# Kernel tuning notes

Measured on AMD Instinct MI355X. Metric: run time of the kernel, lower is better.

The kernel has to match this reference:

```python
import jax, jax.numpy as jnp
import numpy as np

NUM_SPARSE = 26
VOCAB = 100000
EMB = 64
B = 2048
DENSE = 13
NUM_FEA = NUM_SPARSE + 1  # 26 embeddings + bottom-MLP output


def _xavier(key, shape):
    fan_in, fan_out = shape[0], shape[1]
    lim = jnp.sqrt(6.0 / (fan_in + fan_out))
    return jax.random.uniform(key, shape, jnp.float32, -lim, lim)


def setup_inputs() -> dict:
    key = jax.random.key(0)
    ks = jax.random.split(key, 20)
    inp = {
        "dense": jax.random.normal(ks[0], (B, DENSE), jnp.float32),
        "cat_idx": jax.random.randint(ks[1], (B, NUM_SPARSE), 0, VOCAB, jnp.int32),
        # stacked EmbeddingBag tables (all same vocab -> one [26, V, 64] tensor)
        "tables": _xavier(ks[2], (VOCAB, EMB))[None] * jnp.ones((NUM_SPARSE, 1, 1), jnp.float32) * 0
                  + jax.random.normal(ks[3], (NUM_SPARSE, VOCAB, EMB), jnp.float32) * 0.01,
        # bottom MLP: 13 -> 512 -> 256 -> 64
        "bw0": _xavier(ks[4], (DENSE, 512)), "bb0": jnp.zeros((512,), jnp.float32),
        "bw1": _xavier(ks[5], (512, 256)),   "bb1": jnp.zeros((256,), jnp.float32),
        "bw2": _xavier(ks[6], (256, EMB)),   "bb2": jnp.zeros((EMB,), jnp.float32),
        # top MLP: 415 -> 1024 -> 512 -> 256 -> 1
        "tw0": _xavier(ks[7], (EMB + NUM_FEA * (NUM_FEA - 1) // 2, 1024)), "tb0": jnp.zeros((1024,), jnp.float32),
        "tw1": _xavier(ks[8], (1024, 512)),  "tb1": jnp.zeros((512,), jnp.float32),
        "tw2": _xavier(ks[9], (512, 256)),   "tb2": jnp.zeros((256,), jnp.float32),
        "tw3": _xavier(ks[10], (256, 1)),    "tb3": jnp.zeros((1,), jnp.float32),
    }
    return inp


def reference(dense, cat_idx, tables, bw0, bb0, bw1, bb1, bw2, bb2,
              tw0, tb0, tw1, tb1, tw2, tb2, tw3, tb3):
    # bottom MLP on dense features -> [B, EMB]
    h = jax.nn.relu(dense @ bw0 + bb0)
    h = jax.nn.relu(h @ bw1 + bb1)
    bot = jax.nn.relu(h @ bw2 + bb2)

    # EmbeddingBag (single index per bag, sum mode == plain gather): [B, 26, EMB]
    feat_ids = jnp.arange(NUM_SPARSE)[None, :]  # [1, 26]
    emb = tables[feat_ids, cat_idx]             # [B, 26, EMB]

    # dot interaction: batched Gram matrix then lower-triangular gather
    T = jnp.concatenate([bot[:, None, :], emb], axis=1)  # [B, 27, EMB]
    Z = jnp.einsum("bif,bjf->bij", T, T)                  # [B, 27, 27]
    li, lj = np.tril_indices(NUM_FEA, k=-1)               # 351 pairs
    Zflat = Z[:, li, lj]                                  # [B, 351]

    R = jnp.concatenate([bot, Zflat], axis=1)             # [B, 415]

    # top MLP
    r = jax.nn.relu(R @ tw0 + tb0)
    r = jax.nn.relu(r @ tw1 + tb1)
    r = jax.nn.relu(r @ tw2 + tb2)
    out = jax.nn.sigmoid(r @ tw3 + tb3)                   # [B, 1]
    return out
```

## Files before the change

### kernel.cpp

```cpp
#include <hip/hip_runtime.h>
#include <hip/hip_bf16.h>


#define BATCH 2048
#define VOCAB 100000
#define NSPARSE 26
#define NFEA 27
#define NPAIR 351
#define RLD 512

typedef __attribute__((ext_vector_type(8))) __bf16 bf16x8;
typedef __attribute__((ext_vector_type(4))) float f32x4;
typedef __hip_bfloat16 bf16;

#define MFMA16 __builtin_amdgcn_mfma_f32_16x16x32_bf16

#define GLOAD16(g, l)                                                          \
    __builtin_amdgcn_global_load_lds(                                          \
        (const __attribute__((address_space(1))) unsigned int*)(g),            \
        (__attribute__((address_space(3))) unsigned int*)(l), 16, 0, 0)

template<int BK>
__device__ __forceinline__ int swz(int row, int s) {
    return (BK == 128) ? (s ^ (row & 15))
         : (BK == 64)  ? (s ^ (row & 7))
                       : (s ^ ((row >> 1) & 3));
}

__global__ __launch_bounds__(256) void bottom_kernel(
    const float* __restrict__ dense,
    const bf16* __restrict__ bw0t, const float* __restrict__ bb0,
    const bf16* __restrict__ bw1t, const float* __restrict__ bb1,
    const bf16* __restrict__ bw2t, const float* __restrict__ bb2,
    bf16* __restrict__ R)
{
    __shared__ __align__(16) bf16 ds[16 * 32];
    __shared__ __align__(16) bf16 h0s[16 * 512];
    __shared__ __align__(16) bf16 h1s[16 * 256];

    const int t   = threadIdx.x;
    const int b0  = blockIdx.x * 8;
    const int wid = t >> 6, lane = t & 63;
    const int lr  = lane & 15, q = lane >> 4;

    for (int idx = t; idx < 16 * 32; idx += 256) {
        const int r = idx >> 5, c = idx & 31;
        const float v = (r < 8 && c < 13) ? dense[(size_t)(b0 + r) * 13 + c] : 0.f;
        ds[r * 32 + swz<32>(r, c >> 3) * 8 + (c & 7)] = __float2bfloat16(v);
    }
    __syncthreads();

    {
        const bf16x8 af = *(const bf16x8*)&ds[lr * 32 + swz<32>(lr, q) * 8];
        const int n0 = wid * 128;
        f32x4 acc[8] = {};
#pragma unroll
        for (int n = 0; n < 8; ++n) {
            const bf16x8 bv =
                *(const bf16x8*)(bw0t + (size_t)(n0 + n * 16 + lr) * 32 + q * 8);
            acc[n] = MFMA16(af, bv, acc[n], 0, 0, 0);
        }
#pragma unroll
        for (int n = 0; n < 8; ++n) {
            const int col = n0 + n * 16 + lr;
            const float bv = bb0[col];
#pragma unroll
            for (int i = 0; i < 4; ++i) {
                const int row = q * 4 + i;
                const float v = fmaxf(acc[n][i] + bv, 0.f);
                h0s[row * 512 + (((col >> 3) ^ (row & 15)) << 3) + (col & 7)] =
                    __float2bfloat16(v);
            }
        }
    }
    __syncthreads();

    {
        const int n0 = wid * 64;
        const bf16* wp[4];
#pragma unroll
        for (int n = 0; n < 4; ++n)
            wp[n] = bw1t + (size_t)(n0 + n * 16 + lr) * 512 + q * 8;

        f32x4 acc[4] = {};
#pragma unroll 4
        for (int kk = 0; kk < 16; ++kk) {
            const bf16x8 af = *(const bf16x8*)
                &h0s[lr * 512 + (((kk * 4 + q) ^ (lr & 15)) << 3)];
#pragma unroll
            for (int n = 0; n < 4; ++n) {
                const bf16x8 bv = *(const bf16x8*)(wp[n] + kk * 32);
                acc[n] = MFMA16(af, bv, acc[n], 0, 0, 0);
            }
        }
#pragma unroll
        for (int n = 0; n < 4; ++n) {
            const int col = n0 + n * 16 + lr;
            const float bv = bb1[col];
#pragma unroll
            for (int i = 0; i < 4; ++i) {
                const int row = q * 4 + i;
                const float v = fmaxf(acc[n][i] + bv, 0.f);
                h1s[row * 256 + (((col >> 3) ^ (row & 15)) << 3) + (col & 7)] =
                    __float2bfloat16(v);
            }
        }
    }
    __syncthreads();

    {
        const int n0 = wid * 16;
        const bf16* wp = bw2t + (size_t)(n0 + lr) * 256 + q * 8;
        f32x4 acc = {};
#pragma unroll
        for (int kk = 0; kk < 8; ++kk) {
            const bf16x8 af = *(const bf16x8*)
                &h1s[lr * 256 + (((kk * 4 + q) ^ (lr & 15)) << 3)];
            const bf16x8 bv = *(const bf16x8*)(wp + kk * 32);
            acc = MFMA16(af, bv, acc, 0, 0, 0);
        }
        const int col = n0 + lr;
        const float bv = bb2[col];
#pragma unroll
        for (int i = 0; i < 4; ++i) {
            const int row = q * 4 + i;
            if (row < 8) {
                const float v = fmaxf(acc[i] + bv, 0.f);
                R[(size_t)(b0 + row) * RLD + col] = __float2bfloat16(v);
            }
        }
    }
}

template<int BK, int WR, int WC, int MREP, int NREP>
__global__ __launch_bounds__(256) void gemm_bf16(
    const bf16* __restrict__ A, const bf16* __restrict__ Wt,
    const float* __restrict__ bias, bf16* __restrict__ C,
    int M, int N, int K, int ldC)
{
    constexpr int BM    = WR * MREP * 16;
    constexpr int BN    = WC * NREP * 16;
    constexpr int ROWB  = BK * 2;
    constexpr int SLOTS = BK / 8;
    constexpr int KKS   = BK / 32;
    constexpr int PA    = BM * SLOTS / 256;
    constexpr int PB    = BN * SLOTS / 256;

    __shared__ __align__(16) bf16 As[BM * BK];
    __shared__ __align__(16) bf16 Bs[BN * BK];

    const int t   = threadIdx.x;
    const int nbn = N / BN;
    const int bm  = blockIdx.x / nbn;
    const int bn  = blockIdx.x % nbn;
    const int row0 = bm * BM, n0 = bn * BN;

    const int wid  = t >> 6, lane = t & 63;
    const int wr   = wid / WC, wc = wid % WC;
    const int lr   = lane & 15;
    const int q    = lane >> 4;
    const int sslot = t % SLOTS;

    const bf16* Ab[PA];
    const bf16* Bb[PB];
#pragma unroll
    for (int p = 0; p < PA; ++p) {
        const int r = (p * 256 + t) / SLOTS;
        Ab[p] = A + (size_t)(row0 + r) * K + swz<BK>(r, sslot) * 8;
    }
#pragma unroll
    for (int p = 0; p < PB; ++p) {
        const int r = (p * 256 + t) / SLOTS;
        Bb[p] = Wt + (size_t)(n0 + r) * K + swz<BK>(r, sslot) * 8;
    }

    f32x4 acc[MREP][NREP] = {};

    for (int k0 = 0; k0 < K; k0 += BK) {
#pragma unroll
        for (int p = 0; p < PA; ++p)
            GLOAD16(Ab[p] + k0, (char*)As + (p * 256 + t) * 16);
#pragma unroll
        for (int p = 0; p < PB; ++p)
            GLOAD16(Bb[p] + k0, (char*)Bs + (p * 256 + t) * 16);
        __syncthreads();

        bf16x8 af[KKS][MREP], bfr[KKS][NREP];
#pragma unroll
        for (int kk = 0; kk < KKS; ++kk) {
#pragma unroll
            for (int m = 0; m < MREP; ++m) {
                const int r = wr * MREP * 16 + 16 * m + lr;
                af[kk][m] = *(const bf16x8*)((const char*)As + r * ROWB +
                                             swz<BK>(r, kk * 4 + q) * 16);
            }
#pragma unroll
            for (int n = 0; n < NREP; ++n) {
                const int r = wc * NREP * 16 + 16 * n + lr;
                bfr[kk][n] = *(const bf16x8*)((const char*)Bs + r * ROWB +
                                              swz<BK>(r, kk * 4 + q) * 16);
            }
        }
#pragma unroll
        for (int kk = 0; kk < KKS; ++kk)
#pragma unroll
            for (int m = 0; m < MREP; ++m)
#pragma unroll
                for (int n = 0; n < NREP; ++n)
                    acc[m][n] = MFMA16(af[kk][m], bfr[kk][n], acc[m][n], 0, 0, 0);
        __syncthreads();
    }

#pragma unroll
    for (int n = 0; n < NREP; ++n) {
        const int col = n0 + wc * NREP * 16 + 16 * n + lr;
        const float bv = bias[col];
#pragma unroll
        for (int m = 0; m < MREP; ++m) {
#pragma unroll
            for (int i = 0; i < 4; ++i) {
                const int row = row0 + wr * MREP * 16 + 16 * m + q * 4 + i;
                float v = fmaxf(acc[m][n][i] + bv, 0.f);
                C[(size_t)row * ldC + col] = __float2bfloat16(v);
            }
        }
    }
}

__global__ __launch_bounds__(256) void top2_kernel(
    const bf16* __restrict__ A, const bf16* __restrict__ Wt,
    const float* __restrict__ bias, const float* __restrict__ w3,
    const float* __restrict__ b3, float* __restrict__ out)
{
    constexpr int BK = 64, BM = 32, K = 512;
    constexpr int SLOTS = 8, KKS = 2, PA = 1, PB = 8;

    __shared__ __align__(16) bf16 As[BM * BK];
    __shared__ __align__(16) bf16 Bs[256 * BK];
    __shared__ float rsum[BM];

    const int t = threadIdx.x;
    const int row0 = blockIdx.x * BM;
    const int wc = t >> 6, lane = t & 63;
    const int lr = lane & 15, q = lane >> 4;
    const int sslot = t % SLOTS;

    const bf16* Ab[PA];
    const bf16* Bb[PB];
#pragma unroll
    for (int p = 0; p < PA; ++p) {
        const int r = (p * 256 + t) / SLOTS;
        Ab[p] = A + (size_t)(row0 + r) * K + swz<BK>(r, sslot) * 8;
    }
#pragma unroll
    for (int p = 0; p < PB; ++p) {
        const int r = (p * 256 + t) / SLOTS;
        Bb[p] = Wt + (size_t)r * K + swz<BK>(r, sslot) * 8;
    }

    f32x4 acc[2][4] = {};

    for (int k0 = 0; k0 < K; k0 += BK) {
#pragma unroll
        for (int p = 0; p < PA; ++p)
            GLOAD16(Ab[p] + k0, (char*)As + (p * 256 + t) * 16);
#pragma unroll
        for (int p = 0; p < PB; ++p)
            GLOAD16(Bb[p] + k0, (char*)Bs + (p * 256 + t) * 16);
        __syncthreads();

        bf16x8 af[KKS][2], bfr[KKS][4];
#pragma unroll
        for (int kk = 0; kk < KKS; ++kk) {
#pragma unroll
            for (int m = 0; m < 2; ++m) {
                const int r = 16 * m + lr;
                af[kk][m] = *(const bf16x8*)((const char*)As + r * 128 +
                                             swz<BK>(r, kk * 4 + q) * 16);
            }
#pragma unroll
            for (int n = 0; n < 4; ++n) {
                const int r = wc * 64 + 16 * n + lr;
                bfr[kk][n] = *(const bf16x8*)((const char*)Bs + r * 128 +
                                              swz<BK>(r, kk * 4 + q) * 16);
            }
        }
#pragma unroll
        for (int kk = 0; kk < KKS; ++kk)
#pragma unroll
            for (int m = 0; m < 2; ++m)
#pragma unroll
                for (int n = 0; n < 4; ++n)
                    acc[m][n] = MFMA16(af[kk][m], bfr[kk][n], acc[m][n], 0, 0, 0);
        __syncthreads();
    }

    if (t < BM) rsum[t] = 0.f;
    __syncthreads();

#pragma unroll
    for (int m = 0; m < 2; ++m) {
#pragma unroll
        for (int i = 0; i < 4; ++i) {
            float val = 0.f;
#pragma unroll
            for (int n = 0; n < 4; ++n) {
                const int col = wc * 64 + 16 * n + lr;
                val += fmaxf(acc[m][n][i] + bias[col], 0.f) * w3[col];
            }
            val += __shfl_xor(val, 1);
            val += __shfl_xor(val, 2);
            val += __shfl_xor(val, 4);
            val += __shfl_xor(val, 8);
            if (lr == 0) atomicAdd(&rsum[16 * m + q * 4 + i], val);
        }
    }
    __syncthreads();
    if (t < BM)
        out[row0 + t] = 1.f / (1.f + expf(-(rsum[t] + b3[0])));
}

struct WConvArgs {
    const float* src[6];
    bf16*        dst[6];
    int K[6], N[6], Kp[6], t0[7];
};

__global__ __launch_bounds__(256) void wconv_kernel(WConvArgs a)
{
    __shared__ float Ts[32][33];
    int w = 0;
    while (w < 5 && (int)blockIdx.x >= a.t0[w + 1]) ++w;
    const int rel = blockIdx.x - a.t0[w];
    const int K = a.K[w], N = a.N[w], Kp = a.Kp[w];
    const int nbn = N >> 5;
    const int tk = rel / nbn, tn = rel % nbn;
    const int tx = threadIdx.x & 31, ty = threadIdx.x >> 5;

    const float* src = a.src[w];
    bf16* dst = a.dst[w];

#pragma unroll
    for (int rr = 0; rr < 4; ++rr) {
        const int k = tk * 32 + ty + rr * 8;
        const int n = tn * 32 + tx;
        Ts[ty + rr * 8][tx] = (k < K) ? src[(size_t)k * N + n] : 0.f;
    }
    __syncthreads();
#pragma unroll
    for (int rr = 0; rr < 4; ++rr) {
        const int n = tn * 32 + ty + rr * 8;
        const int kp = tk * 32 + tx;
        dst[(size_t)n * Kp + kp] = __float2bfloat16(Ts[tx][ty + rr * 8]);
    }
}

__global__ __launch_bounds__(256) void interact_kernel(
    const int* __restrict__ cat_idx, const float* __restrict__ tables,
    bf16* __restrict__ R)
{
    __shared__ float T[NFEA][64 + 1];

    const int b    = blockIdx.x;
    const int t    = threadIdx.x;
    const int g    = t >> 6;
    const int lane = t & 63;
    bf16* Rrow = R + (size_t)b * RLD;

    for (int f = g; f < NFEA; f += 4) {
        if (f == 0) {
            T[0][lane] = __bfloat162float(Rrow[lane]);
        } else {
            const int j   = f - 1;
            const int idx = cat_idx[b * NSPARSE + j];
            T[f][lane] = tables[((size_t)j * VOCAB + idx) * 64 + lane];
        }
    }
    __syncthreads();

    if (t < RLD - 415) Rrow[415 + t] = __float2bfloat16(0.f);

    for (int p = t; p < NPAIR; p += 256) {
        int i = (int)((1.0f + sqrtf(1.0f + 8.0f * (float)p)) * 0.5f);
        while (i * (i - 1) / 2 > p) --i;
        while ((i + 1) * i / 2 <= p) ++i;
        const int j = p - i * (i - 1) / 2;
        float s = 0.f;
#pragma unroll 16
        for (int k = 0; k < 64; ++k) s += T[i][k] * T[j][k];
        Rrow[64 + p] = __float2bfloat16(s);
    }
}

extern "C" void kernel_launch(void* const* d_in, const int* in_sizes, int n_in,
                              void* d_out, int out_size, void* d_ws, size_t ws_size,
                              hipStream_t stream)
{
    const float* dense   = (const float*)d_in[0];
    const int*   cat_idx = (const int*)  d_in[1];
    const float* tables  = (const float*)d_in[2];
    const float* bw0 = (const float*)d_in[3];
    const float* bb0 = (const float*)d_in[4];
    const float* bw1 = (const float*)d_in[5];
    const float* bb1 = (const float*)d_in[6];
    const float* bw2 = (const float*)d_in[7];
    const float* bb2 = (const float*)d_in[8];
    const float* tw0 = (const float*)d_in[9];
    const float* tb0 = (const float*)d_in[10];
    const float* tw1 = (const float*)d_in[11];
    const float* tb1 = (const float*)d_in[12];
    const float* tw2 = (const float*)d_in[13];
    const float* tb2 = (const float*)d_in[14];
    const float* tw3 = (const float*)d_in[15];
    const float* tb3 = (const float*)d_in[16];

    bf16* p = (bf16*)d_ws;
    bf16* R    = p; p += (size_t)BATCH * RLD;
    bf16* r0   = p; p += (size_t)BATCH * 1024;
    bf16* r1   = p; p += (size_t)BATCH * 512;
    bf16* bw0t = p; p += 512 * 32;
    bf16* bw1t = p; p += 256 * 512;
    bf16* bw2t = p; p += 64 * 256;
    bf16* tw0t = p; p += 1024 * RLD;
    bf16* tw1t = p; p += 512 * 1024;
    bf16* tw2t = p; p += 256 * 512;
    float* out = (float*)d_out;

    WConvArgs wa;
    wa.src[0] = bw0;  wa.dst[0] = bw0t; wa.K[0] = 13;   wa.N[0] = 512;  wa.Kp[0] = 32;
    wa.src[1] = bw1;  wa.dst[1] = bw1t; wa.K[1] = 512;  wa.N[1] = 256;  wa.Kp[1] = 512;
    wa.src[2] = bw2;  wa.dst[2] = bw2t; wa.K[2] = 256;  wa.N[2] = 64;   wa.Kp[2] = 256;
    wa.src[3] = tw0;  wa.dst[3] = tw0t; wa.K[3] = 415;  wa.N[3] = 1024; wa.Kp[3] = RLD;
    wa.src[4] = tw1;  wa.dst[4] = tw1t; wa.K[4] = 1024; wa.N[4] = 512;  wa.Kp[4] = 1024;
    wa.src[5] = tw2;  wa.dst[5] = tw2t; wa.K[5] = 512;  wa.N[5] = 256;  wa.Kp[5] = 512;
    int tiles = 0;
    for (int w = 0; w < 6; ++w) {
        wa.t0[w] = tiles;
        tiles += (wa.Kp[w] >> 5) * (wa.N[w] >> 5);
    }
    wa.t0[6] = tiles;

    wconv_kernel<<<tiles, 256, 0, stream>>>(wa);

    bottom_kernel<<<BATCH / 8, 256, 0, stream>>>(
        dense, bw0t, bb0, bw1t, bb1, bw2t, bb2, R);

    interact_kernel<<<BATCH, 256, 0, stream>>>(cat_idx, tables, R);

    gemm_bf16<128, 2, 2, 1, 2><<<(BATCH / 32) * (1024 / 64), 256, 0, stream>>>(
        R, tw0t, tb0, r0, BATCH, 1024, RLD, 1024);
    gemm_bf16<128, 2, 2, 1, 1><<<(BATCH / 32) * (512 / 32), 256, 0, stream>>>(
        r0, tw1t, tb1, r1, BATCH, 512, 1024, 512);
    top2_kernel<<<BATCH / 32, 256, 0, stream>>>(r1, tw2t, tb2, tw3, tb3, out);
}
```

Before: 59.03 us.

## Fuse embedding gather and dot interaction into bottom MLP kernel

Removes the separate interaction kernel and folds it into the bottom MLP kernel. At kernel start, each block issues asynchronous global-to-LDS loads for its 8 rows' embedding vectors, so the gather overlaps with the MLP matmuls. The pairwise dot products are then computed from bf16 copies in shared memory. This saves one launch and a round trip of the bottom output through global memory, at the cost of much larger LDS use per block (lower occupancy) and bf16 rounding of the embeddings before the dot products.

After: 61.09 us. 1.03x slower.

```diff
diff --git a/kernel.cpp b/kernel.cpp
--- a/kernel.cpp
+++ b/kernel.cpp
@@ -20,6 +20,13 @@
         (const __attribute__((address_space(1))) unsigned int*)(g),            \
         (__attribute__((address_space(3))) unsigned int*)(l), 16, 0, 0)
 
+#define LGKM_BARRIER()                                                         \
+    do {                                                                       \
+        asm volatile("s_waitcnt lgkmcnt(0)" ::: "memory");                     \
+        __builtin_amdgcn_s_barrier();                                          \
+        __builtin_amdgcn_sched_barrier(0);                                     \
+    } while (0)
+
 template<int BK>
 __device__ __forceinline__ int swz(int row, int s) {
     return (BK == 128) ? (s ^ (row & 15))
@@ -28,27 +35,51 @@
 }
 
 __global__ __launch_bounds__(256) void bottom_kernel(
-    const float* __restrict__ dense,
+    const float* __restrict__ dense, const int* __restrict__ cat,
+    const float* __restrict__ tables,
     const bf16* __restrict__ bw0t, const float* __restrict__ bb0,
     const bf16* __restrict__ bw1t, const float* __restrict__ bb1,
     const bf16* __restrict__ bw2t, const float* __restrict__ bb2,
     bf16* __restrict__ R)
 {
+    __shared__ int idxs[8 * NSPARSE];
+    __shared__ __align__(16) float Tg[8 * NSPARSE * 64];
     __shared__ __align__(16) bf16 ds[16 * 32];
     __shared__ __align__(16) bf16 h0s[16 * 512];
     __shared__ __align__(16) bf16 h1s[16 * 256];
+    __shared__ bf16 Tp[8][NFEA][66];
 
     const int t   = threadIdx.x;
     const int b0  = blockIdx.x * 8;
     const int wid = t >> 6, lane = t & 63;
     const int lr  = lane & 15, q = lane >> 4;
 
+    if (t < 8 * NSPARSE) idxs[t] = cat[b0 * NSPARSE + t];
+    __syncthreads();
+
     for (int idx = t; idx < 16 * 32; idx += 256) {
         const int r = idx >> 5, c = idx & 31;
         const float v = (r < 8 && c < 13) ? dense[(size_t)(b0 + r) * 13 + c] : 0.f;
         ds[r * 32 + swz<32>(r, c >> 3) * 8 + (c & 7)] = __float2bfloat16(v);
     }
-    __syncthreads();
+
+#pragma unroll
+    for (int i = 0; i < 13; ++i) {
+        const int g  = wid * 13 + i;
+        const int rf = g * 4 + (lane >> 4);
+        const int r  = rf / NSPARSE, j = rf % NSPARSE;
+        (void)r;
+        const float* src =
+            tables + ((size_t)j * VOCAB + idxs[rf]) * 64 + (lane & 15) * 4;
+        GLOAD16(src, (char*)Tg + ((size_t)g * 64 + lane) * 16);
+    }
+
+    for (int z = t; z < 8 * (RLD - 415); z += 256) {
+        const int r = z / (RLD - 415), c = z % (RLD - 415);
+        R[(size_t)(b0 + r) * RLD + 415 + c] = __float2bfloat16(0.f);
+    }
+
+    LGKM_BARRIER();
 
     {
         const bf16x8 af = *(const bf16x8*)&ds[lr * 32 + swz<32>(lr, q) * 8];
@@ -73,7 +104,7 @@
             }
         }
     }
-    __syncthreads();
+    LGKM_BARRIER();
 
     {
         const int n0 = wid * 64;
@@ -106,7 +137,7 @@
             }
         }
     }
-    __syncthreads();
+    LGKM_BARRIER();
 
     {
         const int n0 = wid * 16;
@@ -126,9 +157,36 @@
             const int row = q * 4 + i;
             if (row < 8) {
                 const float v = fmaxf(acc[i] + bv, 0.f);
-                R[(size_t)(b0 + row) * RLD + col] = __float2bfloat16(v);
-            }
-        }
+                const bf16 hv = __float2bfloat16(v);
+                Tp[row][0][col] = hv;
+                R[(size_t)(b0 + row) * RLD + col] = hv;
+            }
+        }
+    }
+
+    asm volatile("s_waitcnt vmcnt(0) lgkmcnt(0)" ::: "memory");
+    __builtin_amdgcn_s_barrier();
+    __builtin_amdgcn_sched_barrier(0);
+
+    for (int idx = t; idx < 8 * NSPARSE * 64; idx += 256) {
+        const int r   = idx / (NSPARSE * 64);
+        const int rem = idx % (NSPARSE * 64);
+        const int j   = rem >> 6, k = rem & 63;
+        Tp[r][j + 1][k] = __float2bfloat16(Tg[idx]);
+    }
+    LGKM_BARRIER();
+
+    for (int task = t; task < 8 * NPAIR; task += 256) {
+        const int r = task / NPAIR, p = task % NPAIR;
+        int i = (int)((1.0f + sqrtf(1.0f + 8.0f * (float)p)) * 0.5f);
+        while (i * (i - 1) / 2 > p) --i;
+        while ((i + 1) * i / 2 <= p) ++i;
+        const int j = p - i * (i - 1) / 2;
+        float s = 0.f;
+#pragma unroll 16
+        for (int k = 0; k < 64; ++k)
+            s += __bfloat162float(Tp[r][i][k]) * __bfloat162float(Tp[r][j][k]);
+        R[(size_t)(b0 + r) * RLD + 64 + p] = __float2bfloat16(s);
     }
 }
 
@@ -352,43 +410,6 @@
         const int n = tn * 32 + ty + rr * 8;
         const int kp = tk * 32 + tx;
         dst[(size_t)n * Kp + kp] = __float2bfloat16(Ts[tx][ty + rr * 8]);
-    }
-}
-
-__global__ __launch_bounds__(256) void interact_kernel(
-    const int* __restrict__ cat_idx, const float* __restrict__ tables,
-    bf16* __restrict__ R)
-{
-    __shared__ float T[NFEA][64 + 1];
-
-    const int b    = blockIdx.x;
-    const int t    = threadIdx.x;
-    const int g    = t >> 6;
-    const int lane = t & 63;
-    bf16* Rrow = R + (size_t)b * RLD;
-
-    for (int f = g; f < NFEA; f += 4) {
-        if (f == 0) {
-            T[0][lane] = __bfloat162float(Rrow[lane]);
-        } else {
-            const int j   = f - 1;
-            const int idx = cat_idx[b * NSPARSE + j];
-            T[f][lane] = tables[((size_t)j * VOCAB + idx) * 64 + lane];
-        }
-    }
-    __syncthreads();
-
-    if (t < RLD - 415) Rrow[415 + t] = __float2bfloat16(0.f);
-
-    for (int p = t; p < NPAIR; p += 256) {
-        int i = (int)((1.0f + sqrtf(1.0f + 8.0f * (float)p)) * 0.5f);
-        while (i * (i - 1) / 2 > p) --i;
-        while ((i + 1) * i / 2 <= p) ++i;
-        const int j = p - i * (i - 1) / 2;
-        float s = 0.f;
-#pragma unroll 16
-        for (int k = 0; k < 64; ++k) s += T[i][k] * T[j][k];
-        Rrow[64 + p] = __float2bfloat16(s);
     }
 }
 
@@ -443,9 +464,8 @@
     wconv_kernel<<<tiles, 256, 0, stream>>>(wa);
 
     bottom_kernel<<<BATCH / 8, 256, 0, stream>>>(
-        dense, bw0t, bb0, bw1t, bb1, bw2t, bb2, R);
-
-    interact_kernel<<<BATCH, 256, 0, stream>>>(cat_idx, tables, R);
+        dense, cat_idx, tables,
+        bw0t, bb0, bw1t, bb1, bw2t, bb2, R);
 
     gemm_bf16<128, 2, 2, 1, 2><<<(BATCH / 32) * (1024 / 64), 256, 0, stream>>>(
         R, tw0t, tb0, r0, BATCH, 1024, RLD, 1024);
```
